# Optimization experiments

Hardware: AMD Instinct MI355X
Metric: run time of the kernel (lower is better)

## Reference

```python
import jax, jax.numpy as jnp
import numpy as np
import math

B, N, D = 4, 4096, 256


def setup_inputs() -> dict:
    key = jax.random.key(0)
    k0, k1, k2, k3 = jax.random.split(key, 4)
    # kaiming-uniform-like init for the square weight matrices
    bound = math.sqrt(6.0 / D)
    return {
        "x": jax.random.normal(k0, (B, N, D), dtype=jnp.float32),
        "Wq": jax.random.uniform(k1, (D, D), dtype=jnp.float32, minval=-bound, maxval=bound),
        "Wk": jax.random.uniform(k2, (D, D), dtype=jnp.float32, minval=-bound, maxval=bound),
        "Wv": jax.random.uniform(k3, (D, D), dtype=jnp.float32, minval=-bound, maxval=bound),
    }


def reference(x, Wq, Wk, Wv):
    # x: [B, N, D]; W*: [D, D]
    q = x @ Wq.T
    k = x @ Wk.T
    v = x @ Wv.T
    n = x.shape[1]
    d_k = x.shape[2]
    # mask = triu(ones, diagonal=1): 1 strictly above the diagonal.
    # (1 - mask) is 1 on and below the diagonal, so those positions get -1e10
    # (faithful to the original: it masks the diagonal and past, keeps future).
    mask = jnp.triu(jnp.ones((n, n), dtype=x.dtype), k=1)
    scale = jnp.asarray(1.0 / math.sqrt(d_k), dtype=x.dtype)
    s = (jnp.einsum('bnd,bmd->bnm', q, k) - (1.0 - mask) * 1e10) * scale
    # Faithful quirk: softmax over dim=1 (the query/row axis), not the last axis.
    s = jax.nn.softmax(s, axis=1)
    return jnp.einsum('bnm,bmd->bnd', s, v)
```

## Files before the change

kernel.cpp:

```cpp
#include <hip/hip_runtime.h>
#include <hip/hip_bf16.h>


typedef float f32x4 __attribute__((ext_vector_type(4)));
typedef __bf16 bf16x8 __attribute__((ext_vector_type(8)));
typedef __bf16 bf16x4 __attribute__((ext_vector_type(4)));

#define MFMA16(a, b, c) __builtin_amdgcn_mfma_f32_16x16x32_bf16((a), (b), (c), 0, 0, 0)

constexpr int SEQ = 4096;
constexpr int DIM = 256;

__host__ __device__ inline int tri(int x) { return (x * (x + 1)) >> 1; }

__device__ __forceinline__ void gl16(const __bf16* g, __bf16* l) {
  __builtin_amdgcn_global_load_lds((const __attribute__((address_space(1))) void*)g,
                                   (__attribute__((address_space(3))) void*)l, 16, 0, 0);
}

__global__ void k_prep(const float* __restrict__ Wq, const float* __restrict__ Wk,
                       const float* __restrict__ Wv, __bf16* __restrict__ Wb,
                       float* __restrict__ colsum) {
  int i = blockIdx.x * 256 + threadIdx.x;
  if (i < 3 * 65536) {
    const float* src = (i < 65536) ? Wq : (i < 131072 ? Wk : Wv);
    Wb[i] = (__bf16)src[i & 65535];
  }
  if (i < 4 * SEQ) colsum[i] = 0.f;
}

__global__ __launch_bounds__(256, 2) void k_qkv(const float* __restrict__ x,
                                                const __bf16* __restrict__ Wb,
                                                __bf16* __restrict__ Qb,
                                                __bf16* __restrict__ Kb,
                                                __bf16* __restrict__ Vb) {
  __shared__ __bf16 wsh[64][264];
  const int t = threadIdx.x, lane = t & 63, w = t >> 6;
  const int ln = lane & 15, quad = lane >> 4, q8 = quad * 8;
  const int i0 = blockIdx.x * 64;
  bf16x8 xa[8];
#pragma unroll
  for (int kf = 0; kf < 8; ++kf) {
    const float* src = &x[(size_t)(i0 + w * 16 + ln) * DIM + kf * 32 + q8];
    float4 v0 = *(const float4*)&src[0];
    float4 v1 = *(const float4*)&src[4];
    xa[kf] = bf16x8{(__bf16)v0.x, (__bf16)v0.y, (__bf16)v0.z, (__bf16)v0.w,
                    (__bf16)v1.x, (__bf16)v1.y, (__bf16)v1.z, (__bf16)v1.w};
  }
  for (int zj = 0; zj < 12; ++zj) {
    const int z = zj >> 2, j0 = (zj & 3) * 64;
    const __bf16* W = Wb + z * 65536 + j0 * 256;
    bf16x8 stg[8];
#pragma unroll
    for (int i = 0; i < 8; ++i) stg[i] = *(const bf16x8*)&W[(t + i * 256) * 8];
    __syncthreads();
#pragma unroll
    for (int i = 0; i < 8; ++i)
      *(bf16x8*)&wsh[(t >> 5) + i * 8][(t & 31) * 8] = stg[i];
    __syncthreads();
    f32x4 acc[4] = {};
#pragma unroll
    for (int kf = 0; kf < 8; ++kf) {
      bf16x8 bb[4];
#pragma unroll
      for (int tj = 0; tj < 4; ++tj)
        bb[tj] = *(bf16x8*)&wsh[tj * 16 + ln][kf * 32 + q8];
#pragma unroll
      for (int tj = 0; tj < 4; ++tj) acc[tj] = MFMA16(xa[kf], bb[tj], acc[tj]);
    }
    __bf16* Out = (z == 0) ? Qb : (z == 1 ? Kb : Vb);
#pragma unroll
    for (int tj = 0; tj < 4; ++tj)
#pragma unroll
      for (int r = 0; r < 4; ++r) {
        int row = i0 + w * 16 + quad * 4 + r;
        int col = j0 + tj * 16 + ln;
        Out[(size_t)row * DIM + col] = (__bf16)acc[tj][r];
      }
  }
}

__global__ __launch_bounds__(256, 2) void k_scores(const __bf16* __restrict__ Qb,
                                                   const __bf16* __restrict__ Kb,
                                                   __bf16* __restrict__ E,
                                                   float* __restrict__ colsum,
                                                   int mtLo, int triLo, int ntiles) {
  __shared__ __bf16 qsh[2 * 64 * 256];
  const int t = threadIdx.x, lane = t & 63, w = t >> 6;
  const int ln = lane & 15, quad = lane >> 4, q8 = quad * 8;
  const int bid = blockIdx.x;
  const int b = (bid & 7) >> 1;
  const int rest = ((bid >> 3) << 1) | (bid & 1);
  const int mt = mtLo + (rest >> 2);
  const int s = rest & 3;
  if (s > mt) return;
  const int m0 = mt * 64;
  const __bf16* Qp = Qb + (size_t)b * SEQ * DIM;
  const __bf16* Kp = Kb + (size_t)b * SEQ * DIM;
  bf16x8 kb[8];
#pragma unroll
  for (int kf = 0; kf < 8; ++kf)
    kb[kf] = *(const bf16x8*)&Kp[(size_t)(m0 + w * 16 + ln) * DIM + kf * 32 + q8];
  auto stageq = [&](int ncv, int buf) {
    const __bf16* src = Qp + (size_t)ncv * 16384;
#pragma unroll
    for (int i2 = 0; i2 < 8; ++i2) {
      int sl = t + i2 * 256;
      int row = sl >> 5, g = sl & 31;
      gl16(&src[row * 256 + ((g ^ (row & 15)) << 3)], &qsh[buf * 16384 + sl * 8]);
    }
  };
  float csum4[4] = {0.f, 0.f, 0.f, 0.f};
  const int P16 = w * 2 + (quad >> 1);
  const int sub = (quad & 1) * 4;
  int nc = s, cur = 0;
  if (nc <= mt) stageq(nc, 0);
  for (; nc <= mt; nc += 4, cur ^= 1) {
    __syncthreads();
    if (nc + 4 <= mt) stageq(nc + 4, cur ^ 1);
    f32x4 accST[4] = {};
#pragma unroll
    for (int kf = 0; kf < 8; ++kf) {
#pragma unroll
      for (int tn = 0; tn < 4; ++tn) {
        int row = tn * 16 + ln;
        bf16x8 bq = *(const bf16x8*)&qsh[cur * 16384 + row * 256 +
                                         (((kf * 4 + quad) ^ ln) << 3)];
        accST[tn] = MFMA16(kb[kf], bq, accST[tn]);
      }
    }
    __bf16* Et = E + ((size_t)b * ntiles + (tri(mt) - triLo) + nc) * 4096;
#pragma unroll
    for (int tn = 0; tn < 4; ++tn) {
      int nl = tn * 16 + ln;
      int n_g = nc * 64 + nl;
      int mb = m0 + w * 16 + quad * 4;
      bf16x4 pk;
#pragma unroll
      for (int r = 0; r < 4; ++r) {
        float e = (n_g < mb + r) ? __expf(accST[tn][r] * 0.0625f) : 0.f;
        csum4[r] += e;
        pk[r] = (__bf16)e;
      }
      *(bf16x4*)&Et[nl * 64 + ((P16 ^ (nl & 7)) << 3) + sub] = pk;
    }
  }
#pragma unroll
  for (int r = 0; r < 4; ++r) {
    float v = csum4[r];
    v += __shfl_xor(v, 1);
    v += __shfl_xor(v, 2);
    v += __shfl_xor(v, 4);
    v += __shfl_xor(v, 8);
    if (ln == 0) atomicAdd(&colsum[b * SEQ + m0 + w * 16 + quad * 4 + r], v);
  }
}

__global__ void k_vpt(const __bf16* __restrict__ Vb, const float* __restrict__ colsum,
                      __bf16* __restrict__ VpT, int mtLo) {
  __shared__ __bf16 tile[64][72];
  const int t = threadIdx.x;
  const int b = blockIdx.z;
  const int mblk = mtLo + blockIdx.x;
  const int m0 = mblk * 64, d0 = blockIdx.y * 64;
  {
    int row = t >> 2, part = t & 3;
    float cs = colsum[b * SEQ + m0 + row];
    float inv = (m0 + row == 0) ? (1.0f / 4096.0f) : (1.0f / cs);
#pragma unroll
    for (int i = 0; i < 2; ++i) {
      int c = part * 2 + i;
      bf16x8 v = *(const bf16x8*)&Vb[(size_t)(b * SEQ + m0 + row) * DIM + d0 + c * 8];
      bf16x8 o;
#pragma unroll
      for (int j = 0; j < 8; ++j) o[j] = (__bf16)((float)v[j] * inv);
      *(bf16x8*)&tile[row][c * 8] = o;
    }
  }
  __syncthreads();
  {
    int row = t >> 2, part = t & 3;
#pragma unroll
    for (int i = 0; i < 2; ++i) {
      int c = part * 2 + i;
      bf16x8 o;
#pragma unroll
      for (int j = 0; j < 8; ++j) o[j] = tile[c * 8 + j][row];
      *(bf16x8*)&VpT[(size_t)((b * 64 + mblk) * 256 + d0 + row) * 64 +
                     ((c ^ (row & 7)) << 3)] = o;
    }
  }
}

__global__ __launch_bounds__(256, 4) void k_pv(const __bf16* __restrict__ E,
                                               const __bf16* __restrict__ VpT,
                                               const __bf16* __restrict__ Vb,
                                               float* __restrict__ out,
                                               int mtLo, int mtHi, int triLo,
                                               int ntiles) {
  __shared__ __bf16 esh[4 * 32 * 64];
  const int t = threadIdx.x, lane = t & 63, w = t >> 6;
  const int ln = lane & 15, quad = lane >> 4;
  const int bid = blockIdx.x;
  const int b = (bid & 7) >> 1;
  const int idx = ((bid >> 3) << 1) | (bid & 1);
  const int p = idx >> 1, dh = idx & 1;
  const int nt32 = (p & 1) ? (2 * mtHi - 1 - (p >> 1)) : (p >> 1);
  const int nc = nt32 >> 1, half = nt32 & 1;
  const int mtStart = (nc > mtLo) ? nc : mtLo;
  const int n0 = nt32 * 32;
  const __bf16* Vt = VpT + (size_t)b * SEQ * DIM;
  auto stageE = [&](int msv, int buf) {
    const __bf16* ep =
        E + ((size_t)b * ntiles + (tri(msv) - triLo) + nc) * 4096 + half * 2048;
    gl16(&ep[t * 8], &esh[buf * 2048 + t * 8]);
  };
  auto loadbb = [&](bf16x8 (&BB)[2][2], int msv) {
    const __bf16* vp = Vt + (size_t)msv * 16384 + dh * 8192;
#pragma unroll
    for (int kf = 0; kf < 2; ++kf)
#pragma unroll
      for (int td = 0; td < 2; ++td) {
        int rl = w * 32 + td * 16 + ln;
        BB[kf][td] = *(const bf16x8*)&vp[rl * 64 +
                                         (((kf * 4 + quad) ^ (rl & 7)) << 3)];
      }
  };
  f32x4 accO[2][2] = {};
  bf16x8 bbA[2][2], bbB[2][2];
  const int ms0 = mtHi - 1;
  const int T = mtHi - mtStart;
  auto clampm = [&](int m) { return m < mtStart ? mtStart : m; };
  stageE(ms0, 0);
  loadbb(bbA, ms0);
  stageE(clampm(ms0 - 1), 1);
  loadbb(bbB, clampm(ms0 - 1));
  stageE(clampm(ms0 - 2), 2);
  int ms = ms0, bcur = 0;

#define PV_STEP(BBSET)                                                        \
  {                                                                           \
    __builtin_amdgcn_sched_barrier(0);                                        \
    asm volatile("s_waitcnt vmcnt(6)");                                       \
    __builtin_amdgcn_sched_barrier(0);                                        \
    __builtin_amdgcn_s_barrier();                                             \
    __builtin_amdgcn_sched_barrier(0);                                        \
    const __bf16* eb = &esh[bcur * 2048];                                     \
    bf16x8 aa[2][2];                                                          \
    _Pragma("unroll") for (int kf = 0; kf < 2; ++kf)                          \
      _Pragma("unroll") for (int tn = 0; tn < 2; ++tn) {                      \
        int row = tn * 16 + ln;                                               \
        aa[kf][tn] = *(const bf16x8*)&eb[row * 64 +                           \
                                         (((kf * 4 + quad) ^ (row & 7)) << 3)]; \
      }                                                                       \
    __builtin_amdgcn_s_setprio(1);                                            \
    _Pragma("unroll") for (int kf = 0; kf < 2; ++kf)                          \
      _Pragma("unroll") for (int tn = 0; tn < 2; ++tn)                        \
        _Pragma("unroll") for (int td = 0; td < 2; ++td)                      \
          accO[tn][td] = MFMA16(aa[kf][tn], BBSET[kf][td], accO[tn][td]);     \
    __builtin_amdgcn_s_setprio(0);                                            \
    loadbb(BBSET, clampm(ms - 2));           \
    stageE(clampm(ms - 3), (bcur + 3) & 3);               \
    bcur = (bcur + 1) & 3;                                                    \
    --ms;                                                                     \
  }

  int i = 0;
  for (; i + 2 <= T; i += 2) {
    PV_STEP(bbA);
    PV_STEP(bbB);
  }
  if (i < T) PV_STEP(bbA);
#undef PV_STEP
  __builtin_amdgcn_sched_barrier(0);
  asm volatile("s_waitcnt vmcnt(0)");
  __builtin_amdgcn_sched_barrier(0);

  float* Op = out + ((size_t)b << 20);
  const __bf16* V0 = Vb + ((size_t)b << 20);
  const bool init = (nc >= mtLo);
#pragma unroll
  for (int tn = 0; tn < 2; ++tn)
#pragma unroll
    for (int td = 0; td < 2; ++td) {
      int col = dh * 128 + w * 32 + td * 16 + ln;
      float c0 = init ? (float)V0[col] * (1.0f / 4096.0f) : 0.f;
#pragma unroll
      for (int r = 0; r < 4; ++r) {
        int row = n0 + tn * 16 + quad * 4 + r;
        float* pp = &Op[(size_t)row * DIM + col];
        float v = accO[tn][td][r] + c0;
        if (!init) v += *pp;
        *pp = v;
      }
    }
}

extern "C" void kernel_launch(void* const* d_in, const int* in_sizes, int n_in,
                              void* d_out, int out_size, void* d_ws, size_t ws_size,
                              hipStream_t stream) {
  const float* x = (const float*)d_in[0];
  const float* Wq = (const float*)d_in[1];
  const float* Wk = (const float*)d_in[2];
  const float* Wv = (const float*)d_in[3];
  float* out = (float*)d_out;
  char* ws = (char*)d_ws;
  __bf16* Qb = (__bf16*)(ws);
  __bf16* Kb = (__bf16*)(ws + (8u << 20));
  __bf16* Vb = (__bf16*)(ws + (16u << 20));
  __bf16* VpT = (__bf16*)(ws + (24u << 20));
  float* colsum = (float*)(ws + (32u << 20));
  __bf16* Wb = (__bf16*)(ws + (32u << 20) + (1u << 16));
  const size_t base2 = (32u << 20) + (1u << 16) + (384u << 10);
  __bf16* E = (__bf16*)(ws + base2);
  const size_t fullE = (size_t)4 * 2080 * 4096 * sizeof(__bf16);
  int nPass, lo[3], hi[3];
  if (ws_size >= base2 + fullE) {
    nPass = 1; lo[0] = 0; hi[0] = 64;
  } else {
    nPass = 3;
    lo[0] = 0;  hi[0] = 37;
    lo[1] = 37; hi[1] = 53;
    lo[2] = 53; hi[2] = 64;
  }

  k_prep<<<dim3(768), dim3(256), 0, stream>>>(Wq, Wk, Wv, Wb, colsum);
  k_qkv<<<dim3(256), dim3(256), 0, stream>>>(x, Wb, Qb, Kb, Vb);
  for (int p = 0; p < nPass; ++p) {
    const int nmt = hi[p] - lo[p];
    const int triLo = tri(lo[p]);
    const int ntiles = tri(hi[p]) - triLo;
    k_scores<<<dim3(16 * nmt), dim3(256), 0, stream>>>(Qb, Kb, E, colsum,
                                                       lo[p], triLo, ntiles);
    k_vpt<<<dim3(nmt, 4, 4), dim3(256), 0, stream>>>(Vb, colsum, VpT, lo[p]);
    k_pv<<<dim3(16 * hi[p]), dim3(256), 0, stream>>>(E, VpT, Vb, out,
                                                     lo[p], hi[p], triLo, ntiles);
  }
}
```

Baseline: 186.2 us.

## Split PV reduction over m-tile chunks with atomic accumulation into zeroed output

Splits the k_pv reduction over key tiles into chunks of up to 12 m-tiles, launching more blocks so that long triangular rows no longer serialize on a single block. Partial results are combined with float atomicAdd into the output, which k_prep now zeroes first, and the launch-bounds occupancy target goes from 4 to 8. This is meant to improve load balance and occupancy on the triangular workload. In exchange it adds atomic traffic, a full output-zeroing pass, and nondeterministic summation order.

After: 280.6 us. 50.7% more time.

```diff
diff --git a/kernel.cpp b/kernel.cpp
--- a/kernel.cpp
+++ b/kernel.cpp
@@ -20,13 +20,14 @@
 
 __global__ void k_prep(const float* __restrict__ Wq, const float* __restrict__ Wk,
                        const float* __restrict__ Wv, __bf16* __restrict__ Wb,
-                       float* __restrict__ colsum) {
+                       float* __restrict__ colsum, float4* __restrict__ outz) {
   int i = blockIdx.x * 256 + threadIdx.x;
   if (i < 3 * 65536) {
     const float* src = (i < 65536) ? Wq : (i < 131072 ? Wk : Wv);
     Wb[i] = (__bf16)src[i & 65535];
   }
   if (i < 4 * SEQ) colsum[i] = 0.f;
+  if (i < (1 << 20)) outz[i] = float4{0.f, 0.f, 0.f, 0.f};
 }
 
 __global__ __launch_bounds__(256, 2) void k_qkv(const float* __restrict__ x,
@@ -192,22 +193,29 @@
   }
 }
 
-__global__ __launch_bounds__(256, 4) void k_pv(const __bf16* __restrict__ E,
+__global__ __launch_bounds__(256, 8) void k_pv(const __bf16* __restrict__ E,
                                                const __bf16* __restrict__ VpT,
                                                const __bf16* __restrict__ Vb,
                                                float* __restrict__ out,
                                                int mtLo, int mtHi, int triLo,
-                                               int ntiles) {
+                                               int ntiles, int NCH) {
   __shared__ __bf16 esh[4 * 32 * 64];
   const int t = threadIdx.x, lane = t & 63, w = t >> 6;
   const int ln = lane & 15, quad = lane >> 4;
   const int bid = blockIdx.x;
   const int b = (bid & 7) >> 1;
-  const int idx = ((bid >> 3) << 1) | (bid & 1);
-  const int p = idx >> 1, dh = idx & 1;
+  const int rest = ((bid >> 3) << 1) | (bid & 1);
+  const int pr = rest >> 1, dh = rest & 1;
+  const int c = pr % NCH;
+  const int p = pr / NCH;
   const int nt32 = (p & 1) ? (2 * mtHi - 1 - (p >> 1)) : (p >> 1);
   const int nc = nt32 >> 1, half = nt32 & 1;
-  const int mtStart = (nc > mtLo) ? nc : mtLo;
+  const int CS = (mtHi - mtLo + NCH - 1) / NCH;
+  const int mHi_c = mtHi - c * CS;
+  const int mLo_c0 = mHi_c - CS;
+  const int mLo_c = (mLo_c0 > mtLo) ? mLo_c0 : mtLo;
+  const int mtStart = (nc > mLo_c) ? nc : mLo_c;
+  if (mtStart >= mHi_c) return;
   const int n0 = nt32 * 32;
   const __bf16* Vt = VpT + (size_t)b * SEQ * DIM;
   auto stageE = [&](int msv, int buf) {
@@ -228,8 +236,8 @@
   };
   f32x4 accO[2][2] = {};
   bf16x8 bbA[2][2], bbB[2][2];
-  const int ms0 = mtHi - 1;
-  const int T = mtHi - mtStart;
+  const int ms0 = mHi_c - 1;
+  const int T = mHi_c - mtStart;
   auto clampm = [&](int m) { return m < mtStart ? mtStart : m; };
   stageE(ms0, 0);
   loadbb(bbA, ms0);
@@ -278,20 +286,17 @@
 
   float* Op = out + ((size_t)b << 20);
   const __bf16* V0 = Vb + ((size_t)b << 20);
-  const bool init = (nc >= mtLo);
+  const bool addV0 = (nc >= mLo_c) && (nc < mHi_c);
 #pragma unroll
   for (int tn = 0; tn < 2; ++tn)
 #pragma unroll
     for (int td = 0; td < 2; ++td) {
       int col = dh * 128 + w * 32 + td * 16 + ln;
-      float c0 = init ? (float)V0[col] * (1.0f / 4096.0f) : 0.f;
+      float c0 = addV0 ? (float)V0[col] * (1.0f / 4096.0f) : 0.f;
 #pragma unroll
       for (int r = 0; r < 4; ++r) {
         int row = n0 + tn * 16 + quad * 4 + r;
-        float* pp = &Op[(size_t)row * DIM + col];
-        float v = accO[tn][td][r] + c0;
-        if (!init) v += *pp;
-        *pp = v;
+        atomicAdd(&Op[(size_t)row * DIM + col], accO[tn][td][r] + c0);
       }
     }
 }
@@ -324,16 +329,20 @@
     lo[2] = 53; hi[2] = 64;
   }
 
-  k_prep<<<dim3(768), dim3(256), 0, stream>>>(Wq, Wk, Wv, Wb, colsum);
+  k_prep<<<dim3(4096), dim3(256), 0, stream>>>(Wq, Wk, Wv, Wb, colsum,
+                                               (float4*)out);
   k_qkv<<<dim3(256), dim3(256), 0, stream>>>(x, Wb, Qb, Kb, Vb);
   for (int p = 0; p < nPass; ++p) {
     const int nmt = hi[p] - lo[p];
     const int triLo = tri(lo[p]);
     const int ntiles = tri(hi[p]) - triLo;
+    const int span = hi[p] - lo[p];
+    const int nch = (span + 11) / 12;
     k_scores<<<dim3(16 * nmt), dim3(256), 0, stream>>>(Qb, Kb, E, colsum,
                                                        lo[p], triLo, ntiles);
     k_vpt<<<dim3(nmt, 4, 4), dim3(256), 0, stream>>>(Vb, colsum, VpT, lo[p]);
-    k_pv<<<dim3(16 * hi[p]), dim3(256), 0, stream>>>(E, VpT, Vb, out,
-                                                     lo[p], hi[p], triLo, ntiles);
-  }
-}
+    k_pv<<<dim3(16 * hi[p] * nch), dim3(256), 0, stream>>>(E, VpT, Vb, out,
+                                                           lo[p], hi[p], triLo,
+                                                           ntiles, nch);
+  }
+}
```
